# Kernel tuning notes

Hardware: AMD Instinct MI355X
Metric: run time of the kernel (lower is better)

## Reference

```python
import jax, jax.numpy as jnp
import numpy as np

E, H, F, T = 8, 2048, 4096, 16384  # experts, hidden, ffn, total tokens


def setup_inputs() -> dict:
    key = jax.random.key(0)
    k1, k2, k3 = jax.random.split(key, 3)
    std = 1.0 / np.sqrt(H)
    x = jax.random.normal(k1, (T, H), dtype=jnp.float32)
    # trunc_normal_(std=std) ~ normal * std for reference purposes
    w_gate_up = jax.random.normal(k2, (E, 2 * F, H), dtype=jnp.float32) * std
    w_down = jax.random.normal(k3, (E, H, F), dtype=jnp.float32) * std
    # tokens are pre-sorted by expert; uniform routing: T//E tokens per expert
    tokens_per_expert = jnp.full((E,), T // E, dtype=jnp.int64)
    return {"x": x, "w_gate_up": w_gate_up, "w_down": w_down,
            "tokens_per_expert": tokens_per_expert}


def reference(x, w_gate_up, w_down, tokens_per_expert):
    # x: [T, H] sorted by expert; uniform tokens_per_expert => grouped GEMM
    # is a batched GEMM over the expert axis (same math as the per-expert
    # sequential fallback: gate_up = xi @ w_gate_up[i].T, etc.).
    e = w_gate_up.shape[0]
    f = w_down.shape[2]
    xe = x.reshape(e, -1, x.shape[-1])                     # [E, T/E, H]
    gate_up = jnp.einsum('eth,efh->etf', xe, w_gate_up)    # [E, T/E, 2F]
    gate, up = gate_up[..., :f], gate_up[..., f:]
    hidden = jax.nn.silu(gate) * up                        # [E, T/E, F]
    out = jnp.einsum('etf,ehf->eth', hidden, w_down)       # [E, T/E, H]
    return out.reshape(x.shape)
```

## Files before the change

kernel.cpp:

```cpp
#include <hip/hip_runtime.h>
#include <stdint.h>

typedef unsigned short u16;
typedef unsigned int u32;
typedef short bf16x8 __attribute__((ext_vector_type(8)));
typedef float f32x4 __attribute__((ext_vector_type(4)));

#define E_ 8
#define H_ 2048
#define F_ 4096
#define T_ 16384
#define TE_ 2048

#define WAITV(n) asm volatile("s_waitcnt vmcnt(" #n ")" ::: "memory")
#define BARF                       \
  do {                             \
    asm volatile("" ::: "memory"); \
    __builtin_amdgcn_s_barrier();  \
    asm volatile("" ::: "memory"); \
  } while (0)

__device__ __forceinline__ u16 f2bf(float f) {
  u32 u = __builtin_bit_cast(u32, f);
  u32 r = (u + 0x7FFFu + ((u >> 16) & 1u)) >> 16;
  return (u16)r;
}

__device__ __forceinline__ void gload16(const u16* g, u16* l) {
  __builtin_amdgcn_global_load_lds(
      (__attribute__((address_space(1))) void*)g,
      (__attribute__((address_space(3))) void*)l, 16, 0, 0);
}

__device__ __forceinline__ void mfma_b(f32x4& acc, bf16x8 a, bf16x8 b) {
  asm volatile("v_mfma_f32_16x16x32_bf16 %0, %1, %2, %0"
               : "+v"(acc)
               : "v"(a), "v"(b));
}


__global__ __launch_bounds__(256) void cvt_kernel(const float* __restrict__ src,
                                                  u16* __restrict__ dst,
                                                  long n4) {
  long i = (long)blockIdx.x * blockDim.x + threadIdx.x;
  long stride = (long)gridDim.x * blockDim.x;
  const float4* s4 = (const float4*)src;
  uint2* d4 = (uint2*)dst;
  for (; i < n4; i += stride) {
    float4 v = s4[i];
    uint2 o;
    o.x = (u32)f2bf(v.x) | ((u32)f2bf(v.y) << 16);
    o.y = (u32)f2bf(v.z) | ((u32)f2bf(v.w) << 16);
    d4[i] = o;
  }
}


__global__ __launch_bounds__(512, 2) void gemm1_silu(
    const u16* __restrict__ Xb, const u16* __restrict__ Wgu,
    u16* __restrict__ Hid) {
  const int bx = blockIdx.x;
  const int by = blockIdx.y;
  const int z = blockIdx.z;
  Xb += (size_t)z * TE_ * H_;
  Wgu += (size_t)z * 2 * F_ * H_;
  Hid += (size_t)z * TE_ * F_;

  const int tid = threadIdx.x, w = tid >> 6, lane = tid & 63;
  const int rq = w >> 1, ch = w & 1;
  const int r15 = lane & 15, g4 = lane >> 4;

  __shared__ __attribute__((aligned(16))) u16 lds[65536];

  const u16* gA = Xb + (size_t)(by * 256 + r15) * H_ + g4 * 8;
  const u16* gBg = Wgu + (size_t)(bx * 128 + r15) * H_ + g4 * 8;
  const u16* gBu = Wgu + (size_t)(F_ + bx * 128 + r15) * H_ + g4 * 8;

  auto stage = [&](int t, int buf) {
    u16* L = lds + buf * 32768;
    const int kb = t * 64;
#pragma unroll
    for (int i = 0; i < 4; ++i) {
      const int c = i * 8 + w, rg = c >> 1, ks = c & 1;
      gload16(gA + (size_t)(rg * 16) * H_ + kb + ks * 32,
              L + c * 512 + lane * 8);
    }
#pragma unroll
    for (int i = 0; i < 2; ++i) {
      const int c = i * 8 + w, rg = c >> 1, ks = c & 1;
      gload16(gBg + (size_t)(rg * 16) * H_ + kb + ks * 32,
              L + 16384 + c * 512 + lane * 8);
    }
#pragma unroll
    for (int i = 2; i < 4; ++i) {
      const int c = i * 8 + w, rg = (c >> 1) - 8, ks = c & 1;
      gload16(gBu + (size_t)(rg * 16) * H_ + kb + ks * 32,
              L + 16384 + c * 512 + lane * 8);
    }
  };

  f32x4 accG[4][4] = {};
  f32x4 accU[4][4] = {};

  auto comp = [&](int buf) {
    const u16* LA = lds + buf * 32768 + lane * 8;
    const u16* LB = LA + 16384;
#pragma unroll
    for (int ks = 0; ks < 2; ++ks) {
      bf16x8 a[4], bg[4], bu[4];
#pragma unroll
      for (int mi = 0; mi < 4; ++mi)
        a[mi] = *(const bf16x8*)&LA[((rq * 4 + mi) * 2 + ks) * 512];
#pragma unroll
      for (int ni = 0; ni < 4; ++ni) {
        bg[ni] = *(const bf16x8*)&LB[((ch * 4 + ni) * 2 + ks) * 512];
        bu[ni] = *(const bf16x8*)&LB[((8 + ch * 4 + ni) * 2 + ks) * 512];
      }
      __builtin_amdgcn_s_setprio(1);
#pragma unroll
      for (int mi = 0; mi < 4; ++mi)
#pragma unroll
        for (int ni = 0; ni < 4; ++ni) {
          mfma_b(accG[mi][ni], a[mi], bg[ni]);
          mfma_b(accU[mi][ni], a[mi], bu[ni]);
        }
      __builtin_amdgcn_s_setprio(0);
    }
  };

  const int NT = H_ / 64;
  stage(0, 0);
  stage(1, 1);
  for (int t = 0; t < NT - 1; ++t) {
    WAITV(8);
    BARF;
    comp(t & 1);
    BARF;
    if (t + 2 < NT) stage(t + 2, t & 1);
  }
  WAITV(0);
  BARF;
  comp((NT - 1) & 1);

  const int row0 = by * 256 + rq * 64 + g4 * 4;
  const int col0 = bx * 128 + ch * 64 + r15;
#pragma unroll
  for (int mi = 0; mi < 4; ++mi)
#pragma unroll
    for (int ni = 0; ni < 4; ++ni)
#pragma unroll
      for (int j = 0; j < 4; ++j) {
        float g = accG[mi][ni][j];
        float u = accU[mi][ni][j];
        float h = (g / (1.f + __expf(-g))) * u;
        Hid[(size_t)(row0 + mi * 16 + j) * F_ + col0 + ni * 16] = f2bf(h);
      }
}


__global__ __launch_bounds__(512) void gemm2_down(const u16* __restrict__ Hd,
                                                  const u16* __restrict__ Wd,
                                                  float* __restrict__ Out,
                                                  long sH, long sW, long sO) {
  const int z = blockIdx.z;
  Hd += (long)z * sH;
  Wd += (long)z * sW;
  Out += (long)z * sO;

  const int bx = blockIdx.x;
  const int by = blockIdx.y;
  const int tid = threadIdx.x;
  const int w = tid >> 6;
  const int lane = tid & 63;
  const int wr = w >> 1, wc = w & 1;

  __shared__ __attribute__((aligned(16))) u16 lds[3 * 24576];

  const int srow = (w << 3) + (lane >> 3);
  const int scol = (((lane & 7) ^ (lane >> 3)) << 3);
  const u16* gA = Hd + (size_t)((by << 8) + srow) * F_ + scol;
  const u16* gB = Wd + (size_t)((bx << 7) + srow) * F_ + scol;

  auto stage = [&](int t, int buf) {
    u16* L = &lds[buf * 24576];
    const int ko = t << 6;
    const int wb = w << 3;
#pragma unroll
    for (int i = 0; i < 4; ++i)
      gload16(gA + (size_t)(i * 64) * F_ + ko, &L[((i << 6) + wb) << 6]);
#pragma unroll
    for (int i = 0; i < 2; ++i)
      gload16(gB + (size_t)(i * 64) * F_ + ko,
              &L[16384 + (((i << 6) + wb) << 6)]);
  };

  f32x4 acc[4][4] = {};
  const int fr = lane & 15, q = lane >> 4, l7 = lane & 7;

  auto comp = [&](int buf) {
    const u16* L = &lds[buf * 24576];
    bf16x8 a[4][2], b[4][2];
#pragma unroll
    for (int ni = 0; ni < 4; ++ni)
#pragma unroll
      for (int ks = 0; ks < 2; ++ks) {
        int r = (wc << 6) + (ni << 4) + fr;
        b[ni][ks] =
            *(const bf16x8*)&L[16384 + (r << 6) + ((((ks << 2) + q) ^ l7) << 3)];
      }
#pragma unroll
    for (int mi = 0; mi < 4; ++mi)
#pragma unroll
      for (int ks = 0; ks < 2; ++ks) {
        int r = (wr << 6) + (mi << 4) + fr;
        a[mi][ks] = *(const bf16x8*)&L[(r << 6) + ((((ks << 2) + q) ^ l7) << 3)];
      }
    __builtin_amdgcn_s_setprio(1);
#pragma unroll
    for (int mi = 0; mi < 4; ++mi)
#pragma unroll
      for (int ni = 0; ni < 4; ++ni)
#pragma unroll
        for (int ks = 0; ks < 2; ++ks)
          mfma_b(acc[mi][ni], a[mi][ks], b[ni][ks]);
    __builtin_amdgcn_s_setprio(0);
  };

  const int NT = F_ / 64;
  stage(0, 0);
  stage(1, 1);
  int b0 = 0, b1 = 1, b2 = 2;
  for (int t = 0; t < NT - 2; ++t) {
    stage(t + 2, b2);
    WAITV(12);
    BARF;
    comp(b0);
    BARF;
    int tmp = b0; b0 = b1; b1 = b2; b2 = tmp;
  }
  WAITV(6); BARF;
  comp(b0);
  BARF;
  WAITV(0); BARF;
  comp(b1);

  const int row0 = (by << 8) + (wr << 6) + (q << 2);
  const int col0 = (bx << 7) + (wc << 6) + fr;
#pragma unroll
  for (int mi = 0; mi < 4; ++mi)
#pragma unroll
    for (int ni = 0; ni < 4; ++ni)
#pragma unroll
      for (int j = 0; j < 4; ++j)
        Out[(size_t)(row0 + (mi << 4) + j) * H_ + col0 + (ni << 4)] =
            acc[mi][ni][j];
}


extern "C" void kernel_launch(void* const* d_in, const int* in_sizes, int n_in,
                              void* d_out, int out_size, void* d_ws,
                              size_t ws_size, hipStream_t stream) {
  (void)in_sizes;
  (void)n_in;
  (void)out_size;
  const float* x = (const float*)d_in[0];
  const float* wgu = (const float*)d_in[1];
  const float* wdn = (const float*)d_in[2];
  float* out = (float*)d_out;
  u16* ws = (u16*)d_ws;

  const size_t xbN = (size_t)T_ * H_;
  const size_t wguN = (size_t)E_ * 2 * F_ * H_;
  const size_t wdnN = (size_t)E_ * H_ * F_;
  const size_t hidN = (size_t)T_ * F_;
  const size_t fullBytes = (xbN + wguN + wdnN + hidN) * 2;

  dim3 cblk(256), gblk(512);

  if (ws_size >= fullBytes) {
    u16* xb = ws;
    u16* wgub = xb + xbN;
    u16* wdnb = wgub + wguN;
    u16* hid = wdnb + wdnN;
    cvt_kernel<<<2048, cblk, 0, stream>>>(x, xb, (long)(xbN / 4));
    cvt_kernel<<<4096, cblk, 0, stream>>>(wgu, wgub, (long)(wguN / 4));
    cvt_kernel<<<4096, cblk, 0, stream>>>(wdn, wdnb, (long)(wdnN / 4));
    gemm1_silu<<<dim3(F_ / 128, TE_ / 256, E_), gblk, 0, stream>>>(xb, wgub,
                                                                   hid);
    gemm2_down<<<dim3(H_ / 128, TE_ / 256, E_), gblk, 0, stream>>>(
        hid, wdnb, out, (long)TE_ * F_, (long)H_ * F_, (long)TE_ * H_);
  } else {
    u16* xb = ws;
    u16* wgub = xb + (size_t)TE_ * H_;
    u16* wdnb = wgub + (size_t)2 * F_ * H_;
    u16* hid = wdnb + (size_t)H_ * F_;
    for (int e = 0; e < E_; ++e) {
      cvt_kernel<<<1024, cblk, 0, stream>>>(x + (size_t)e * TE_ * H_, xb,
                                            (long)((size_t)TE_ * H_ / 4));
      cvt_kernel<<<2048, cblk, 0, stream>>>(wgu + (size_t)e * 2 * F_ * H_, wgub,
                                            (long)((size_t)2 * F_ * H_ / 4));
      cvt_kernel<<<2048, cblk, 0, stream>>>(wdn + (size_t)e * H_ * F_, wdnb,
                                            (long)((size_t)H_ * F_ / 4));
      gemm1_silu<<<dim3(F_ / 128, TE_ / 256, 1), gblk, 0, stream>>>(xb, wgub,
                                                                    hid);
      gemm2_down<<<dim3(H_ / 128, TE_ / 256, 1), gblk, 0, stream>>>(
          hid, wdnb, out + (size_t)e * TE_ * H_, 0, 0, 0);
    }
  }
}
```

Measured before the change: 1.186 ms.

## Shrink gemm1 tiles with XOR-swizzled LDS layout and fuse conversion kernels

Rewrites gemm1_silu to use 256-thread blocks computing 128x64 output tiles (gate and up), down from 512 threads and 256x128 tiles. LDS now holds row-major 64-wide K slices with an XOR swizzle to avoid bank conflicts. The three fp32-to-bf16 conversion launches are merged into one kernel over the concatenated workspace. Smaller tiles raise block count and occupancy but lower per-block data reuse and increase global traffic.

```diff
diff --git a/kernel.cpp b/kernel.cpp
--- a/kernel.cpp
+++ b/kernel.cpp
@@ -39,15 +39,28 @@
 }
 
 
-__global__ __launch_bounds__(256) void cvt_kernel(const float* __restrict__ src,
-                                                  u16* __restrict__ dst,
-                                                  long n4) {
+__global__ __launch_bounds__(256) void cvt3_kernel(
+    const float* __restrict__ s0, const float* __restrict__ s1,
+    const float* __restrict__ s2, u16* __restrict__ dst, long n0, long n1,
+    long n2) {
   long i = (long)blockIdx.x * blockDim.x + threadIdx.x;
   long stride = (long)gridDim.x * blockDim.x;
-  const float4* s4 = (const float4*)src;
+  const long ntot = n0 + n1 + n2;
   uint2* d4 = (uint2*)dst;
-  for (; i < n4; i += stride) {
-    float4 v = s4[i];
+  for (; i < ntot; i += stride) {
+    const float4* s4;
+    long j;
+    if (i < n0) {
+      s4 = (const float4*)s0;
+      j = i;
+    } else if (i < n0 + n1) {
+      s4 = (const float4*)s1;
+      j = i - n0;
+    } else {
+      s4 = (const float4*)s2;
+      j = i - n0 - n1;
+    }
+    float4 v = s4[j];
     uint2 o;
     o.x = (u32)f2bf(v.x) | ((u32)f2bf(v.y) << 16);
     o.y = (u32)f2bf(v.z) | ((u32)f2bf(v.w) << 16);
@@ -56,71 +69,69 @@
 }
 
 
-__global__ __launch_bounds__(512, 2) void gemm1_silu(
+__global__ __launch_bounds__(256, 2) void gemm1_silu(
     const u16* __restrict__ Xb, const u16* __restrict__ Wgu,
-    u16* __restrict__ Hid) {
+    u16* __restrict__ Hid, long sX, long sW, long sH) {
+  const int z = blockIdx.z;
+  Xb += (long)z * sX;
+  Wgu += (long)z * sW;
+  Hid += (long)z * sH;
+
   const int bx = blockIdx.x;
   const int by = blockIdx.y;
-  const int z = blockIdx.z;
-  Xb += (size_t)z * TE_ * H_;
-  Wgu += (size_t)z * 2 * F_ * H_;
-  Hid += (size_t)z * TE_ * F_;
-
-  const int tid = threadIdx.x, w = tid >> 6, lane = tid & 63;
-  const int rq = w >> 1, ch = w & 1;
-  const int r15 = lane & 15, g4 = lane >> 4;
-
-  __shared__ __attribute__((aligned(16))) u16 lds[65536];
-
-  const u16* gA = Xb + (size_t)(by * 256 + r15) * H_ + g4 * 8;
-  const u16* gBg = Wgu + (size_t)(bx * 128 + r15) * H_ + g4 * 8;
-  const u16* gBu = Wgu + (size_t)(F_ + bx * 128 + r15) * H_ + g4 * 8;
+  const int tid = threadIdx.x;
+  const int w = tid >> 6;
+  const int lane = tid & 63;
+  const int wr = w >> 1, wc = w & 1;
+  const int fr = lane & 15, q = lane >> 4, l7 = lane & 7;
+
+  __shared__ __attribute__((aligned(16))) u16 lds[2 * 16384];
+
+  const int srow8 = lane >> 3;
+  const int sgran = (lane & 7) ^ (lane >> 3);
+  const u16* gA = Xb + (size_t)(by * 128 + srow8) * H_ + sgran * 8;
+  const u16* gBg = Wgu + (size_t)(bx * 64 + srow8) * H_ + sgran * 8;
+  const u16* gBu = gBg + (size_t)F_ * H_;
 
   auto stage = [&](int t, int buf) {
-    u16* L = lds + buf * 32768;
-    const int kb = t * 64;
+    u16* L = lds + buf * 16384;
+    const int ko = t * 64;
 #pragma unroll
     for (int i = 0; i < 4; ++i) {
-      const int c = i * 8 + w, rg = c >> 1, ks = c & 1;
-      gload16(gA + (size_t)(rg * 16) * H_ + kb + ks * 32,
-              L + c * 512 + lane * 8);
+      const int c = i * 4 + w;
+      gload16(gA + (size_t)(c * 8) * H_ + ko, L + c * 512 + lane * 8);
     }
 #pragma unroll
     for (int i = 0; i < 2; ++i) {
-      const int c = i * 8 + w, rg = c >> 1, ks = c & 1;
-      gload16(gBg + (size_t)(rg * 16) * H_ + kb + ks * 32,
-              L + 16384 + c * 512 + lane * 8);
-    }
-#pragma unroll
-    for (int i = 2; i < 4; ++i) {
-      const int c = i * 8 + w, rg = (c >> 1) - 8, ks = c & 1;
-      gload16(gBu + (size_t)(rg * 16) * H_ + kb + ks * 32,
-              L + 16384 + c * 512 + lane * 8);
+      const int c = i * 4 + w;
+      gload16(gBg + (size_t)(c * 8) * H_ + ko, L + 8192 + c * 512 + lane * 8);
+      gload16(gBu + (size_t)(c * 8) * H_ + ko, L + 12288 + c * 512 + lane * 8);
     }
   };
 
-  f32x4 accG[4][4] = {};
-  f32x4 accU[4][4] = {};
+  f32x4 accG[4][2] = {};
+  f32x4 accU[4][2] = {};
 
   auto comp = [&](int buf) {
-    const u16* LA = lds + buf * 32768 + lane * 8;
-    const u16* LB = LA + 16384;
+    const u16* L = lds + buf * 16384;
 #pragma unroll
     for (int ks = 0; ks < 2; ++ks) {
-      bf16x8 a[4], bg[4], bu[4];
+      const int seg = (((ks << 2) + q) ^ l7) << 3;
+      bf16x8 a[4], bg[2], bu[2];
 #pragma unroll
       for (int mi = 0; mi < 4; ++mi)
-        a[mi] = *(const bf16x8*)&LA[((rq * 4 + mi) * 2 + ks) * 512];
-#pragma unroll
-      for (int ni = 0; ni < 4; ++ni) {
-        bg[ni] = *(const bf16x8*)&LB[((ch * 4 + ni) * 2 + ks) * 512];
-        bu[ni] = *(const bf16x8*)&LB[((8 + ch * 4 + ni) * 2 + ks) * 512];
+        a[mi] = *(const bf16x8*)&L[(wr * 64 + mi * 16 + fr) * 64 + seg];
+#pragma unroll
+      for (int ni = 0; ni < 2; ++ni) {
+        bg[ni] = *(const bf16x8*)&L[8192 + (wc * 32 + ni * 16 + fr) * 64 + seg];
+        bu[ni] =
+            *(const bf16x8*)&L[12288 + (wc * 32 + ni * 16 + fr) * 64 + seg];
       }
       __builtin_amdgcn_s_setprio(1);
 #pragma unroll
       for (int mi = 0; mi < 4; ++mi)
 #pragma unroll
-        for (int ni = 0; ni < 4; ++ni) {
+        for (int ni = 0; ni < 2; ++ni) {
           mfma_b(accG[mi][ni], a[mi], bg[ni]);
           mfma_b(accU[mi][ni], a[mi], bu[ni]);
         }
@@ -142,12 +153,12 @@
   BARF;
   comp((NT - 1) & 1);
 
-  const int row0 = by * 256 + rq * 64 + g4 * 4;
-  const int col0 = bx * 128 + ch * 64 + r15;
+  const int row0 = by * 128 + wr * 64 + q * 4;
+  const int col0 = bx * 64 + wc * 32 + fr;
 #pragma unroll
   for (int mi = 0; mi < 4; ++mi)
 #pragma unroll
-    for (int ni = 0; ni < 4; ++ni)
+    for (int ni = 0; ni < 2; ++ni)
 #pragma unroll
       for (int j = 0; j < 4; ++j) {
         float g = accG[mi][ni][j];
@@ -275,19 +286,18 @@
   const size_t hidN = (size_t)T_ * F_;
   const size_t fullBytes = (xbN + wguN + wdnN + hidN) * 2;
 
-  dim3 cblk(256), gblk(512);
+  dim3 cblk(256), g1blk(256), g2blk(512);
 
   if (ws_size >= fullBytes) {
     u16* xb = ws;
     u16* wgub = xb + xbN;
     u16* wdnb = wgub + wguN;
     u16* hid = wdnb + wdnN;
-    cvt_kernel<<<2048, cblk, 0, stream>>>(x, xb, (long)(xbN / 4));
-    cvt_kernel<<<4096, cblk, 0, stream>>>(wgu, wgub, (long)(wguN / 4));
-    cvt_kernel<<<4096, cblk, 0, stream>>>(wdn, wdnb, (long)(wdnN / 4));
-    gemm1_silu<<<dim3(F_ / 128, TE_ / 256, E_), gblk, 0, stream>>>(xb, wgub,
-                                                                   hid);
-    gemm2_down<<<dim3(H_ / 128, TE_ / 256, E_), gblk, 0, stream>>>(
+    cvt3_kernel<<<4096, cblk, 0, stream>>>(x, wgu, wdn, ws, (long)(xbN / 4),
+                                           (long)(wguN / 4), (long)(wdnN / 4));
+    gemm1_silu<<<dim3(F_ / 64, TE_ / 128, E_), g1blk, 0, stream>>>(
+        xb, wgub, hid, (long)TE_ * H_, (long)2 * F_ * H_, (long)TE_ * F_);
+    gemm2_down<<<dim3(H_ / 128, TE_ / 256, E_), g2blk, 0, stream>>>(
         hid, wdnb, out, (long)TE_ * F_, (long)H_ * F_, (long)TE_ * H_);
   } else {
     u16* xb = ws;
@@ -295,15 +305,14 @@
     u16* wdnb = wgub + (size_t)2 * F_ * H_;
     u16* hid = wdnb + (size_t)H_ * F_;
     for (int e = 0; e < E_; ++e) {
-      cvt_kernel<<<1024, cblk, 0, stream>>>(x + (size_t)e * TE_ * H_, xb,
-                                            (long)((size_t)TE_ * H_ / 4));
-      cvt_kernel<<<2048, cblk, 0, stream>>>(wgu + (size_t)e * 2 * F_ * H_, wgub,
-                                            (long)((size_t)2 * F_ * H_ / 4));
-      cvt_kernel<<<2048, cblk, 0, stream>>>(wdn + (size_t)e * H_ * F_, wdnb,
-                                            (long)((size_t)H_ * F_ / 4));
-      gemm1_silu<<<dim3(F_ / 128, TE_ / 256, 1), gblk, 0, stream>>>(xb, wgub,
-                                                                    hid);
-      gemm2_down<<<dim3(H_ / 128, TE_ / 256, 1), gblk, 0, stream>>>(
+      cvt3_kernel<<<2048, cblk, 0, stream>>>(
+          x + (size_t)e * TE_ * H_, wgu + (size_t)e * 2 * F_ * H_,
+          wdn + (size_t)e * H_ * F_, ws, (long)((size_t)TE_ * H_ / 4),
+          (long)((size_t)2 * F_ * H_ / 4), (long)((size_t)H_ * F_ / 4));
+      gemm1_silu<<<dim3(F_ / 64, TE_ / 128, 1), g1blk, 0, stream>>>(xb, wgub,
+                                                                    hid, 0, 0,
+                                                                    0);
+      gemm2_down<<<dim3(H_ / 128, TE_ / 256, 1), g2blk, 0, stream>>>(
           hid, wdnb, out + (size_t)e * TE_ * H_, 0, 0, 0);
     }
   }
```

New measurement: 1.097 ms. -7.5%, faster.
